# Optimization experiments

Hardware: AMD Instinct MI355X
Metric: run time of the kernel (lower is better)

The kernel has to match this reference:

```python
import jax, jax.numpy as jnp
import numpy as np
from jax import lax

B_, C_, H_, W_ = 4, 128, 64, 64
D_INNER, D_STATE, DT_RANK, D_CONV = 256, 16, 8, 4


def setup_inputs() -> dict:
    ks = jax.random.split(jax.random.key(0), 12)
    def rn(k, shape, fan_in):
        return jax.random.normal(k, shape, jnp.float32) * (fan_in ** -0.5)
    return {
        "x": jax.random.normal(ks[0], (B_, C_, H_, W_), jnp.float32),
        "proj_w": rn(ks[1], (C_, C_), C_),
        "in_proj_w": rn(ks[2], (2 * D_INNER, C_), C_),
        "conv_w": rn(ks[3], (D_INNER, 1, D_CONV), D_CONV),
        "conv_b": jax.random.normal(ks[4], (D_INNER,), jnp.float32) * 0.02,
        "x_proj_w": rn(ks[5], (DT_RANK + 2 * D_STATE, D_INNER), D_INNER),
        "dt_proj_w": rn(ks[6], (D_INNER, DT_RANK), DT_RANK),
        "dt_proj_b": jax.random.normal(ks[7], (D_INNER,), jnp.float32) * 0.1,
        "A_log": jax.random.uniform(ks[8], (D_INNER, D_STATE), jnp.float32),
        "D": jax.random.normal(ks[9], (D_INNER,), jnp.float32),
        "out_proj_w": rn(ks[10], (C_, D_INNER), D_INNER),
    }


def _mamba2d(x, proj_w, in_proj_w, conv_w, conv_b, x_proj_w, dt_proj_w, dt_proj_b, A_log, D, out_proj_w):
    b, c, h, w = x.shape
    L = h * w
    # 1x1 conv projection then flatten to sequence (b, L, c)
    u = jnp.einsum('oc,bchw->bohw', proj_w, x).reshape(b, c, L).transpose(0, 2, 1)
    # in_proj -> x, z gates
    xz = u @ in_proj_w.T                      # (b, L, 2*d_inner)
    xs, zg = xz[..., :D_INNER], xz[..., D_INNER:]
    # causal depthwise conv1d over sequence
    xt = xs.transpose(0, 2, 1)                # (b, d_inner, L)
    xt = lax.conv_general_dilated(xt, conv_w, window_strides=(1,),
                                  padding=[(D_CONV - 1, 0)],
                                  feature_group_count=D_INNER)
    xc = jax.nn.silu(xt + conv_b[None, :, None]).transpose(0, 2, 1)  # (b, L, d_inner)
    # input-dependent SSM params
    x_dbl = xc @ x_proj_w.T                   # (b, L, dt_rank + 2*d_state)
    dt_r = x_dbl[..., :DT_RANK]
    Bm = x_dbl[..., DT_RANK:DT_RANK + D_STATE]
    Cm = x_dbl[..., DT_RANK + D_STATE:]
    delta = jax.nn.softplus(dt_r @ dt_proj_w.T + dt_proj_b)  # (b, L, d_inner)
    A = -jnp.exp(A_log)                       # (d_inner, d_state)

    def step(hprev, inp):
        dt_t, B_t, C_t, x_t = inp             # (b,d), (b,n), (b,n), (b,d)
        dA = jnp.exp(dt_t[:, :, None] * A)    # (b, d, n)
        hn = dA * hprev + (dt_t * x_t)[:, :, None] * B_t[:, None, :]
        y = jnp.einsum('bdn,bn->bd', hn, C_t)
        return hn, y

    h0 = jnp.zeros((b, D_INNER, D_STATE), xc.dtype)
    _, ys = lax.scan(step, h0, (delta.transpose(1, 0, 2), Bm.transpose(1, 0, 2),
                                Cm.transpose(1, 0, 2), xc.transpose(1, 0, 2)))
    y = ys.transpose(1, 0, 2) + xc * D        # (b, L, d_inner) + skip
    y = y * jax.nn.silu(zg)                   # output gating
    out = y @ out_proj_w.T                    # (b, L, c)
    return out.transpose(0, 2, 1).reshape(b, c, h, w) + x


def reference(x, proj_w, in_proj_w, conv_w, conv_b, x_proj_w, dt_proj_w, dt_proj_b, A_log, D, out_proj_w):
    return _mamba2d(x, proj_w, in_proj_w, conv_w, conv_b, x_proj_w, dt_proj_w, dt_proj_b, A_log, D, out_proj_w)
```

## Files before the change

kernel.cpp:

```cpp
#include <hip/hip_runtime.h>


#define NCHUNK 128
#define CLEN 32

using s16x8 = __attribute__((ext_vector_type(8))) short;
using f32x4 = __attribute__((ext_vector_type(4))) float;

__device__ inline unsigned short f2bf(float f) {
  unsigned u = __float_as_uint(f);
  u = u + 0x7FFF + ((u >> 16) & 1);
  return (unsigned short)(u >> 16);
}

__global__ void prep_kernel(const float* __restrict__ proj_w,
                            const float* __restrict__ in_proj_w,
                            const float* __restrict__ x_proj_w,
                            const float* __restrict__ A_log,
                            unsigned short* __restrict__ W2b,
                            float* __restrict__ wT,
                            float* __restrict__ Aneg) {
  int idx = blockIdx.x * blockDim.x + threadIdx.x;
  if (idx < 512 * 128) {
    int o = idx >> 7, c = idx & 127;
    float acc = 0.f;
    #pragma unroll 4
    for (int i = 0; i < 128; ++i)
      acc += in_proj_w[o * 128 + i] * proj_w[i * 128 + c];
    W2b[idx] = f2bf(acc);
  } else if (idx < 512 * 128 + 256 * 40) {
    int t = idx - 512 * 128;
    int k = t / 40, j = t % 40;
    wT[t] = x_proj_w[j * 256 + k];
  } else if (idx < 512 * 128 + 256 * 40 + 256 * 16) {
    int t = idx - (512 * 128 + 256 * 40);
    Aneg[t] = -__expf(A_log[t]);
  }
}

__global__ __launch_bounds__(256, 1) void gemm_xz_kernel(
    const float* __restrict__ x, const unsigned short* __restrict__ W2b,
    float* __restrict__ xz) {
  __shared__ __align__(16) unsigned short At[128 * 128];
  __shared__ __align__(16) unsigned short Bt[256 * 128];
  int m0 = (blockIdx.x >> 1) * 128;
  int o0 = (blockIdx.x & 1) * 256;
  int b  = m0 >> 12;
  int l0 = m0 & 4095;
  int t = threadIdx.x;
  #pragma unroll
  for (int j = 0; j < 16; ++j) {
    int flat = t + j * 256;
    int cr = flat >> 5, lq = (flat & 31) << 2;
    float4 v = *reinterpret_cast<const float4*>(
        &x[((size_t)(b * 128 + cr)) * 4096 + l0 + lq]);
    float vv[4] = {v.x, v.y, v.z, v.w};
    #pragma unroll
    for (int e = 0; e < 4; ++e) {
      int l = lq + e;
      int g = (cr >> 3) ^ ((l & 7) << 1);
      At[l * 128 + g * 8 + (cr & 7)] = f2bf(vv[e]);
    }
  }
  #pragma unroll
  for (int j = 0; j < 16; ++j) {
    int flat = t + j * 256;
    int row = flat >> 4, gB = flat & 15;
    s16x8 v = *reinterpret_cast<const s16x8*>(&W2b[(size_t)(o0 + row) * 128 + gB * 8]);
    int g = gB ^ ((row & 7) << 1);
    *reinterpret_cast<s16x8*>(&Bt[row * 128 + g * 8]) = v;
  }
  __syncthreads();
  int ln = t & 63, wave = t >> 6;
  int wm = wave & 1, wn = wave >> 1;
  f32x4 acc[4][8] = {};
  #pragma unroll
  for (int ks = 0; ks < 4; ++ks) {
    int gk = ks * 4 + (ln >> 4);
    s16x8 a[4], bb[8];
    #pragma unroll
    for (int mi = 0; mi < 4; ++mi) {
      int lr = wm * 64 + mi * 16 + (ln & 15);
      a[mi] = *reinterpret_cast<const s16x8*>(&At[lr * 128 + (gk ^ ((lr & 7) << 1)) * 8]);
    }
    #pragma unroll
    for (int ni = 0; ni < 8; ++ni) {
      int orow = wn * 128 + ni * 16 + (ln & 15);
      bb[ni] = *reinterpret_cast<const s16x8*>(&Bt[orow * 128 + (gk ^ ((orow & 7) << 1)) * 8]);
    }
    #pragma unroll
    for (int mi = 0; mi < 4; ++mi)
      #pragma unroll
      for (int ni = 0; ni < 8; ++ni)
        acc[mi][ni] = __builtin_amdgcn_mfma_f32_16x16x32_bf16(a[mi], bb[ni], acc[mi][ni], 0, 0, 0);
  }
  #pragma unroll
  for (int mi = 0; mi < 4; ++mi)
    #pragma unroll
    for (int ni = 0; ni < 8; ++ni)
      #pragma unroll
      for (int r = 0; r < 4; ++r) {
        int row = wm * 64 + mi * 16 + (ln >> 4) * 4 + r;
        int col = wn * 128 + ni * 16 + (ln & 15);
        xz[(size_t)(m0 + row) * 512 + o0 + col] = acc[mi][ni][r];
      }
}

__global__ __launch_bounds__(256) void conv_silu_kernel(
    const float* __restrict__ xz, const float* __restrict__ conv_w,
    const float* __restrict__ conv_b, float* __restrict__ xc) {
  int bl0 = blockIdx.x * 8;
  int d = threadIdx.x;
  int l0 = bl0 & 4095;
  float w0 = conv_w[d * 4 + 0], w1 = conv_w[d * 4 + 1];
  float w2 = conv_w[d * 4 + 2], w3 = conv_w[d * 4 + 3];
  float cb = conv_b[d];
  float xm1 = (l0 >= 1) ? xz[(size_t)(bl0 - 1) * 512 + d] : 0.f;
  float xm2 = (l0 >= 2) ? xz[(size_t)(bl0 - 2) * 512 + d] : 0.f;
  float xm3 = (l0 >= 3) ? xz[(size_t)(bl0 - 3) * 512 + d] : 0.f;
  #pragma unroll
  for (int r = 0; r < 8; ++r) {
    size_t bl = bl0 + r;
    float x0 = xz[bl * 512 + d];
    float acc = cb + w3 * x0 + w2 * xm1 + w1 * xm2 + w0 * xm3;
    float s = acc * (1.f / (1.f + __expf(-acc)));
    xc[bl * 256 + d] = s;
    xm3 = xm2; xm2 = xm1; xm1 = x0;
  }
}

__global__ __launch_bounds__(256) void xdbl_scan1_kernel(
    const float* __restrict__ xc, const float* __restrict__ wT,
    const float* __restrict__ dt_proj_w, const float* __restrict__ dt_proj_b,
    const float* __restrict__ Aneg,
    float* __restrict__ BC, float* __restrict__ dlt,
    float* __restrict__ Ssum, float* __restrict__ chH) {
  __shared__ __align__(16) float lx[32][256];
  __shared__ float sdtr[32][8];
  __shared__ __align__(16) float lBC[32][32];
  int bc = blockIdx.x;
  int b = bc >> 7, c = bc & 127;
  int m0 = bc * 32;
  int tid = threadIdx.x;
  #pragma unroll
  for (int jj = 0; jj < 8; ++jj) {
    int i = tid + jj * 256;
    int row = i >> 6, colq = (i & 63) << 2;
    *reinterpret_cast<float4*>(&lx[row][colq]) =
        *reinterpret_cast<const float4*>(&xc[(size_t)(m0 + row) * 256 + colq]);
  }
  __syncthreads();
  {
    int j = tid & 63, g = tid >> 6;
    bool act = j < 40;
    float acc[8] = {};
    for (int k = 0; k < 256; ++k) {
      float w = act ? wT[k * 40 + j] : 0.f;
      #pragma unroll
      for (int i = 0; i < 8; ++i)
        acc[i] += lx[g * 8 + i][k] * w;
    }
    if (j < 8) {
      #pragma unroll
      for (int i = 0; i < 8; ++i)
        sdtr[g * 8 + i][j] = acc[i];
    } else if (j < 40) {
      #pragma unroll
      for (int i = 0; i < 8; ++i) {
        BC[(size_t)(m0 + g * 8 + i) * 32 + (j - 8)] = acc[i];
        lBC[g * 8 + i][j - 8] = acc[i];
      }
    }
  }
  __syncthreads();
  int d = tid;
  float dl_r[32];
  {
    float wrow[8];
    #pragma unroll
    for (int r = 0; r < 8; ++r) wrow[r] = dt_proj_w[d * 8 + r];
    float bb = dt_proj_b[d];
    #pragma unroll 4
    for (int r = 0; r < 32; ++r) {
      float a = bb;
      #pragma unroll
      for (int q = 0; q < 8; ++q) a += sdtr[r][q] * wrow[q];
      float sp = fmaxf(a, 0.f) + __logf(1.f + __expf(-fabsf(a)));
      dl_r[r] = sp;
      dlt[(size_t)(m0 + r) * 256 + d] = sp;
    }
  }
  float An[16];
  #pragma unroll
  for (int q = 0; q < 4; ++q)
    *reinterpret_cast<float4*>(&An[q * 4]) =
        *reinterpret_cast<const float4*>(&Aneg[d * 16 + q * 4]);
  float h[16] = {};
  float S = 0.f;
  #pragma unroll
  for (int t = 0; t < CLEN; ++t) {
    float dlv = dl_r[t];
    float dlx = dlv * lx[t][d];
    S += dlv;
    float4 B0 = *reinterpret_cast<const float4*>(&lBC[t][0]);
    float4 B1 = *reinterpret_cast<const float4*>(&lBC[t][4]);
    float4 B2 = *reinterpret_cast<const float4*>(&lBC[t][8]);
    float4 B3 = *reinterpret_cast<const float4*>(&lBC[t][12]);
    float Bv[16] = {B0.x,B0.y,B0.z,B0.w,B1.x,B1.y,B1.z,B1.w,
                    B2.x,B2.y,B2.z,B2.w,B3.x,B3.y,B3.z,B3.w};
    #pragma unroll
    for (int n = 0; n < 16; ++n)
      h[n] = __expf(dlv * An[n]) * h[n] + dlx * Bv[n];
  }
  int p = b * 256 + d;
  Ssum[c * 1024 + p] = S;
  size_t base = ((size_t)(c * 1024 + p)) * 16;
  #pragma unroll
  for (int q = 0; q < 4; ++q) {
    float4 v{h[q*4+0], h[q*4+1], h[q*4+2], h[q*4+3]};
    *reinterpret_cast<float4*>(&chH[base + q * 4]) = v;
  }
}

__global__ void scan2_kernel(const float* __restrict__ Aneg,
                             const float* __restrict__ Ssum,
                             const float* __restrict__ chH,
                             float* __restrict__ chS) {
  int q = blockIdx.x * blockDim.x + threadIdx.x;
  int p = q >> 4, n = q & 15;
  int d = p & 255;
  float An = Aneg[d * 16 + n];
  float h = 0.f;
  #pragma unroll 8
  for (int c = 0; c < NCHUNK; ++c) {
    size_t idx = ((size_t)(c * 1024 + p)) * 16 + n;
    float S = Ssum[c * 1024 + p];
    float hl = chH[idx];
    chS[idx] = h;
    h = __expf(An * S) * h + hl;
  }
}

__global__ __launch_bounds__(256) void scan3_kernel(
    const float* dlt, const float* __restrict__ xc,
    const float* __restrict__ BC, const float* __restrict__ Aneg,
    const float* __restrict__ chS, const float* __restrict__ Dvec,
    const float* __restrict__ xz, float* y2) {
  __shared__ __align__(16) float lBC[CLEN][32];
  int bc = blockIdx.x;
  int b = bc >> 7, c = bc & 127;
  int d = threadIdx.x;
  int bl0 = b * 4096 + c * CLEN;
  {
    int t = threadIdx.x >> 3, q = (threadIdx.x & 7) << 2;
    *reinterpret_cast<float4*>(&lBC[t][q]) =
        *reinterpret_cast<const float4*>(&BC[(size_t)(bl0 + t) * 32 + q]);
  }
  float An[16];
  #pragma unroll
  for (int q = 0; q < 4; ++q)
    *reinterpret_cast<float4*>(&An[q * 4]) =
        *reinterpret_cast<const float4*>(&Aneg[d * 16 + q * 4]);
  int p = b * 256 + d;
  float h[16];
  {
    size_t base = ((size_t)(c * 1024 + p)) * 16;
    #pragma unroll
    for (int q = 0; q < 4; ++q) {
      float4 v = *reinterpret_cast<const float4*>(&chS[base + q * 4]);
      h[q*4+0] = v.x; h[q*4+1] = v.y; h[q*4+2] = v.z; h[q*4+3] = v.w;
    }
  }
  float dl[CLEN], xv[CLEN], zv[CLEN];
  #pragma unroll
  for (int t = 0; t < CLEN; ++t) {
    dl[t] = dlt[(size_t)(bl0 + t) * 256 + d];
    xv[t] = xc[(size_t)(bl0 + t) * 256 + d];
    zv[t] = xz[(size_t)(bl0 + t) * 512 + 256 + d];
  }
  float Dd = Dvec[d];
  __syncthreads();
  #pragma unroll
  for (int t = 0; t < CLEN; ++t) {
    float dlv = dl[t];
    float xvv = xv[t];
    float dlx = dlv * xvv;
    float4 B0 = *reinterpret_cast<const float4*>(&lBC[t][0]);
    float4 B1 = *reinterpret_cast<const float4*>(&lBC[t][4]);
    float4 B2 = *reinterpret_cast<const float4*>(&lBC[t][8]);
    float4 B3 = *reinterpret_cast<const float4*>(&lBC[t][12]);
    float4 C0 = *reinterpret_cast<const float4*>(&lBC[t][16]);
    float4 C1 = *reinterpret_cast<const float4*>(&lBC[t][20]);
    float4 C2 = *reinterpret_cast<const float4*>(&lBC[t][24]);
    float4 C3 = *reinterpret_cast<const float4*>(&lBC[t][28]);
    float Bv[16] = {B0.x,B0.y,B0.z,B0.w,B1.x,B1.y,B1.z,B1.w,
                    B2.x,B2.y,B2.z,B2.w,B3.x,B3.y,B3.z,B3.w};
    float Cv[16] = {C0.x,C0.y,C0.z,C0.w,C1.x,C1.y,C1.z,C1.w,
                    C2.x,C2.y,C2.z,C2.w,C3.x,C3.y,C3.z,C3.w};
    float y = 0.f;
    #pragma unroll
    for (int n = 0; n < 16; ++n) {
      h[n] = __expf(dlv * An[n]) * h[n] + dlx * Bv[n];
      y += h[n] * Cv[n];
    }
    float z = zv[t];
    float sil = z * (1.f / (1.f + __expf(-z)));
    y2[(size_t)(bl0 + t) * 256 + d] = (y + xvv * Dd) * sil;
  }
}

__global__ __launch_bounds__(256) void gemm_out_kernel(
    const float* __restrict__ y2, const float* __restrict__ Wout,
    const float* __restrict__ x, float* __restrict__ out) {
  __shared__ __align__(16) float ys[64][68];
  __shared__ __align__(16) float ws2[64][132];
  int m0 = blockIdx.x * 64;
  int b = m0 >> 12;
  int l0 = m0 & 4095;
  int tid = threadIdx.x;
  int tx = tid & 7;
  int ty = tid >> 3;
  float acc[8][4] = {};
  for (int kc = 0; kc < 256; kc += 64) {
    #pragma unroll
    for (int jj = 0; jj < 4; ++jj) {
      int i = tid + jj * 256;
      int ml = i >> 4, kq = (i & 15) << 2;
      float4 v = *reinterpret_cast<const float4*>(
          &y2[(size_t)(m0 + ml) * 256 + kc + kq]);
      ys[kq + 0][ml] = v.x; ys[kq + 1][ml] = v.y;
      ys[kq + 2][ml] = v.z; ys[kq + 3][ml] = v.w;
    }
    #pragma unroll
    for (int jj = 0; jj < 8; ++jj) {
      int i = tid + jj * 256;
      int cc = i >> 4, kq = (i & 15) << 2;
      float4 v = *reinterpret_cast<const float4*>(&Wout[(size_t)cc * 256 + kc + kq]);
      ws2[kq + 0][cc] = v.x; ws2[kq + 1][cc] = v.y;
      ws2[kq + 2][cc] = v.z; ws2[kq + 3][cc] = v.w;
    }
    __syncthreads();
    for (int kk = 0; kk < 64; ++kk) {
      float4 xa = *reinterpret_cast<const float4*>(&ys[kk][tx * 8]);
      float4 xb = *reinterpret_cast<const float4*>(&ys[kk][tx * 8 + 4]);
      float4 wa = *reinterpret_cast<const float4*>(&ws2[kk][ty * 4]);
      float xv[8] = {xa.x, xa.y, xa.z, xa.w, xb.x, xb.y, xb.z, xb.w};
      float wv[4] = {wa.x, wa.y, wa.z, wa.w};
      #pragma unroll
      for (int i2 = 0; i2 < 8; ++i2)
        #pragma unroll
        for (int j2 = 0; j2 < 4; ++j2)
          acc[i2][j2] += xv[i2] * wv[j2];
    }
    __syncthreads();
  }
  #pragma unroll
  for (int j2 = 0; j2 < 4; ++j2) {
    int cc = ty * 4 + j2;
    size_t base = ((size_t)(b * 128 + cc)) * 4096 + l0 + tx * 8;
    float4 xa = *reinterpret_cast<const float4*>(&x[base]);
    float4 xb = *reinterpret_cast<const float4*>(&x[base + 4]);
    float4 r0{acc[0][j2] + xa.x, acc[1][j2] + xa.y, acc[2][j2] + xa.z, acc[3][j2] + xa.w};
    float4 r1{acc[4][j2] + xb.x, acc[5][j2] + xb.y, acc[6][j2] + xb.z, acc[7][j2] + xb.w};
    *reinterpret_cast<float4*>(&out[base]) = r0;
    *reinterpret_cast<float4*>(&out[base + 4]) = r1;
  }
}

extern "C" void kernel_launch(void* const* d_in, const int* in_sizes, int n_in,
                              void* d_out, int out_size, void* d_ws, size_t ws_size,
                              hipStream_t stream) {
  const float* x         = (const float*)d_in[0];
  const float* proj_w    = (const float*)d_in[1];
  const float* in_proj_w = (const float*)d_in[2];
  const float* conv_w    = (const float*)d_in[3];
  const float* conv_b    = (const float*)d_in[4];
  const float* x_proj_w  = (const float*)d_in[5];
  const float* dt_proj_w = (const float*)d_in[6];
  const float* dt_proj_b = (const float*)d_in[7];
  const float* A_log     = (const float*)d_in[8];
  const float* Dvec      = (const float*)d_in[9];
  const float* out_proj_w= (const float*)d_in[10];

  float* ws   = (float*)d_ws;
  float* wT   = ws;
  float* Aneg = wT + 10240;
  unsigned short* W2b = (unsigned short*)(Aneg + 4096);
  float* xz   = Aneg + 4096 + 32768;
  float* xc   = xz + 8388608;
  float* BC   = xc + 4194304;
  float* dlt  = BC + 524288;
  float* Ssum = dlt + 4194304;
  float* chH  = Ssum + 131072;
  float* chS  = chH + 2097152;
  float* y2   = dlt;
  float* out  = (float*)d_out;

  prep_kernel<<<312, 256, 0, stream>>>(proj_w, in_proj_w, x_proj_w, A_log, W2b, wT, Aneg);
  gemm_xz_kernel<<<256, 256, 0, stream>>>(x, W2b, xz);
  conv_silu_kernel<<<2048, 256, 0, stream>>>(xz, conv_w, conv_b, xc);
  xdbl_scan1_kernel<<<512, 256, 0, stream>>>(xc, wT, dt_proj_w, dt_proj_b, Aneg,
                                             BC, dlt, Ssum, chH);
  scan2_kernel<<<64, 256, 0, stream>>>(Aneg, Ssum, chH, chS);
  scan3_kernel<<<512, 256, 0, stream>>>(dlt, xc, BC, Aneg, chS, Dvec, xz, y2);
  gemm_out_kernel<<<256, 256, 0, stream>>>(y2, out_proj_w, x, out);
}
```

Before: 220.1 us.

## Move x_proj and out_proj GEMMs to bf16 MFMA and recompute delta in scans

Splits the x_proj projection out of the first scan kernel into a bf16 MFMA GEMM, which needs a bf16 copy of xc written by the conv kernel. The out_proj GEMM moves from an fp32 FMA tile loop to MFMA on bf16 y2 and bf16 weights. Delta is no longer stored; both scan passes recompute it from the small dt_r values, which removes a large fp32 intermediate write and read. The cost is an extra launch, extra bf16 rounding on activations, and duplicated softplus work in both scans.

```diff
diff --git a/kernel.cpp b/kernel.cpp
--- a/kernel.cpp
+++ b/kernel.cpp
@@ -16,24 +16,29 @@
 __global__ void prep_kernel(const float* __restrict__ proj_w,
                             const float* __restrict__ in_proj_w,
                             const float* __restrict__ x_proj_w,
+                            const float* __restrict__ out_proj_w,
                             const float* __restrict__ A_log,
                             unsigned short* __restrict__ W2b,
-                            float* __restrict__ wT,
+                            unsigned short* __restrict__ wTb48,
+                            unsigned short* __restrict__ Woutb,
                             float* __restrict__ Aneg) {
   int idx = blockIdx.x * blockDim.x + threadIdx.x;
-  if (idx < 512 * 128) {
+  if (idx < 65536) {
     int o = idx >> 7, c = idx & 127;
     float acc = 0.f;
     #pragma unroll 4
     for (int i = 0; i < 128; ++i)
       acc += in_proj_w[o * 128 + i] * proj_w[i * 128 + c];
     W2b[idx] = f2bf(acc);
-  } else if (idx < 512 * 128 + 256 * 40) {
-    int t = idx - 512 * 128;
-    int k = t / 40, j = t % 40;
-    wT[t] = x_proj_w[j * 256 + k];
-  } else if (idx < 512 * 128 + 256 * 40 + 256 * 16) {
-    int t = idx - (512 * 128 + 256 * 40);
+  } else if (idx < 65536 + 12288) {
+    int t = idx - 65536;
+    int j = t >> 8, k = t & 255;
+    wTb48[t] = (j < 40) ? f2bf(x_proj_w[j * 256 + k]) : (unsigned short)0;
+  } else if (idx < 65536 + 12288 + 32768) {
+    int t = idx - (65536 + 12288);
+    Woutb[t] = f2bf(out_proj_w[t]);
+  } else if (idx < 65536 + 12288 + 32768 + 4096) {
+    int t = idx - (65536 + 12288 + 32768);
     Aneg[t] = -__expf(A_log[t]);
   }
 }
@@ -108,7 +113,8 @@
 
 __global__ __launch_bounds__(256) void conv_silu_kernel(
     const float* __restrict__ xz, const float* __restrict__ conv_w,
-    const float* __restrict__ conv_b, float* __restrict__ xc) {
+    const float* __restrict__ conv_b, float* __restrict__ xc,
+    unsigned short* __restrict__ xcb) {
   int bl0 = blockIdx.x * 8;
   int d = threadIdx.x;
   int l0 = bl0 & 4095;
@@ -125,83 +131,106 @@
     float acc = cb + w3 * x0 + w2 * xm1 + w1 * xm2 + w0 * xm3;
     float s = acc * (1.f / (1.f + __expf(-acc)));
     xc[bl * 256 + d] = s;
+    xcb[bl * 256 + d] = f2bf(s);
     xm3 = xm2; xm2 = xm1; xm1 = x0;
   }
 }
 
-__global__ __launch_bounds__(256) void xdbl_scan1_kernel(
-    const float* __restrict__ xc, const float* __restrict__ wT,
+__global__ __launch_bounds__(256) void xdbl_mfma_kernel(
+    const unsigned short* __restrict__ xcb, const unsigned short* __restrict__ wTb48,
+    float* __restrict__ xdbl48) {
+  __shared__ __align__(16) unsigned short At[64 * 256];
+  __shared__ __align__(16) unsigned short Bt[48 * 256];
+  int m0 = blockIdx.x * 64;
+  int t = threadIdx.x;
+  #pragma unroll
+  for (int it = 0; it < 8; ++it) {
+    int f = t + it * 256;
+    int row = f >> 5, g0 = f & 31;
+    s16x8 v = *reinterpret_cast<const s16x8*>(&xcb[(size_t)(m0 + row) * 256 + g0 * 8]);
+    int g = g0 ^ ((row & 7) << 1);
+    *reinterpret_cast<s16x8*>(&At[row * 256 + g * 8]) = v;
+  }
+  #pragma unroll
+  for (int it = 0; it < 6; ++it) {
+    int f = t + it * 256;
+    int row = f >> 5, g0 = f & 31;
+    s16x8 v = *reinterpret_cast<const s16x8*>(&wTb48[(size_t)row * 256 + g0 * 8]);
+    int g = g0 ^ ((row & 7) << 1);
+    *reinterpret_cast<s16x8*>(&Bt[row * 256 + g * 8]) = v;
+  }
+  __syncthreads();
+  int ln = t & 63, wm = t >> 6;
+  f32x4 acc[3] = {};
+  #pragma unroll
+  for (int ks = 0; ks < 8; ++ks) {
+    int gk = ks * 4 + (ln >> 4);
+    int ar = wm * 16 + (ln & 15);
+    s16x8 a = *reinterpret_cast<const s16x8*>(&At[ar * 256 + (gk ^ ((ar & 7) << 1)) * 8]);
+    #pragma unroll
+    for (int nt = 0; nt < 3; ++nt) {
+      int br = nt * 16 + (ln & 15);
+      s16x8 bb = *reinterpret_cast<const s16x8*>(&Bt[br * 256 + (gk ^ ((br & 7) << 1)) * 8]);
+      acc[nt] = __builtin_amdgcn_mfma_f32_16x16x32_bf16(a, bb, acc[nt], 0, 0, 0);
+    }
+  }
+  #pragma unroll
+  for (int nt = 0; nt < 3; ++nt)
+    #pragma unroll
+    for (int r = 0; r < 4; ++r) {
+      int row = m0 + wm * 16 + (ln >> 4) * 4 + r;
+      xdbl48[(size_t)row * 48 + nt * 16 + (ln & 15)] = acc[nt][r];
+    }
+}
+
+__global__ __launch_bounds__(256) void scan1_kernel(
+    const float* __restrict__ xc, const float* __restrict__ xdbl48,
     const float* __restrict__ dt_proj_w, const float* __restrict__ dt_proj_b,
     const float* __restrict__ Aneg,
-    float* __restrict__ BC, float* __restrict__ dlt,
     float* __restrict__ Ssum, float* __restrict__ chH) {
-  __shared__ __align__(16) float lx[32][256];
-  __shared__ float sdtr[32][8];
-  __shared__ __align__(16) float lBC[32][32];
+  __shared__ __align__(16) float lBC[CLEN][32];
+  __shared__ __align__(16) float sdtr[CLEN][8];
   int bc = blockIdx.x;
-  int b = bc >> 7, c = bc & 127;
-  int m0 = bc * 32;
+  int b = bc >> 7;
+  int bl0 = bc * 32;
   int tid = threadIdx.x;
-  #pragma unroll
-  for (int jj = 0; jj < 8; ++jj) {
-    int i = tid + jj * 256;
-    int row = i >> 6, colq = (i & 63) << 2;
-    *reinterpret_cast<float4*>(&lx[row][colq]) =
-        *reinterpret_cast<const float4*>(&xc[(size_t)(m0 + row) * 256 + colq]);
-  }
-  __syncthreads();
   {
-    int j = tid & 63, g = tid >> 6;
-    bool act = j < 40;
-    float acc[8] = {};
-    for (int k = 0; k < 256; ++k) {
-      float w = act ? wT[k * 40 + j] : 0.f;
-      #pragma unroll
-      for (int i = 0; i < 8; ++i)
-        acc[i] += lx[g * 8 + i][k] * w;
-    }
-    if (j < 8) {
-      #pragma unroll
-      for (int i = 0; i < 8; ++i)
-        sdtr[g * 8 + i][j] = acc[i];
-    } else if (j < 40) {
-      #pragma unroll
-      for (int i = 0; i < 8; ++i) {
-        BC[(size_t)(m0 + g * 8 + i) * 32 + (j - 8)] = acc[i];
-        lBC[g * 8 + i][j - 8] = acc[i];
-      }
-    }
-  }
-  __syncthreads();
+    int t0 = tid >> 3, q = (tid & 7) << 2;
+    *reinterpret_cast<float4*>(&lBC[t0][q]) =
+        *reinterpret_cast<const float4*>(&xdbl48[(size_t)(bl0 + t0) * 48 + 8 + q]);
+    if (tid < 64) {
+      int t1 = tid >> 1, q1 = (tid & 1) << 2;
+      *reinterpret_cast<float4*>(&sdtr[t1][q1]) =
+          *reinterpret_cast<const float4*>(&xdbl48[(size_t)(bl0 + t1) * 48 + q1]);
+    }
+  }
   int d = tid;
-  float dl_r[32];
-  {
-    float wrow[8];
-    #pragma unroll
-    for (int r = 0; r < 8; ++r) wrow[r] = dt_proj_w[d * 8 + r];
-    float bb = dt_proj_b[d];
-    #pragma unroll 4
-    for (int r = 0; r < 32; ++r) {
-      float a = bb;
-      #pragma unroll
-      for (int q = 0; q < 8; ++q) a += sdtr[r][q] * wrow[q];
-      float sp = fmaxf(a, 0.f) + __logf(1.f + __expf(-fabsf(a)));
-      dl_r[r] = sp;
-      dlt[(size_t)(m0 + r) * 256 + d] = sp;
-    }
-  }
+  float wrow[8];
+  *reinterpret_cast<float4*>(&wrow[0]) =
+      *reinterpret_cast<const float4*>(&dt_proj_w[d * 8]);
+  *reinterpret_cast<float4*>(&wrow[4]) =
+      *reinterpret_cast<const float4*>(&dt_proj_w[d * 8 + 4]);
+  float bb = dt_proj_b[d];
   float An[16];
   #pragma unroll
   for (int q = 0; q < 4; ++q)
     *reinterpret_cast<float4*>(&An[q * 4]) =
         *reinterpret_cast<const float4*>(&Aneg[d * 16 + q * 4]);
+  float xv[CLEN];
+  #pragma unroll
+  for (int t = 0; t < CLEN; ++t)
+    xv[t] = xc[(size_t)(bl0 + t) * 256 + d];
+  __syncthreads();
   float h[16] = {};
   float S = 0.f;
   #pragma unroll
   for (int t = 0; t < CLEN; ++t) {
-    float dlv = dl_r[t];
-    float dlx = dlv * lx[t][d];
+    float a = bb;
+    #pragma unroll
+    for (int q = 0; q < 8; ++q) a += sdtr[t][q] * wrow[q];
+    float dlv = fmaxf(a, 0.f) + __logf(1.f + __expf(-fabsf(a)));
     S += dlv;
+    float dlx = dlv * xv[t];
     float4 B0 = *reinterpret_cast<const float4*>(&lBC[t][0]);
     float4 B1 = *reinterpret_cast<const float4*>(&lBC[t][4]);
     float4 B2 = *reinterpret_cast<const float4*>(&lBC[t][8]);
@@ -212,6 +241,7 @@
     for (int n = 0; n < 16; ++n)
       h[n] = __expf(dlv * An[n]) * h[n] + dlx * Bv[n];
   }
+  int c = bc & 127;
   int p = b * 256 + d;
   Ssum[c * 1024 + p] = S;
   size_t base = ((size_t)(c * 1024 + p)) * 16;
@@ -242,20 +272,34 @@
 }
 
 __global__ __launch_bounds__(256) void scan3_kernel(
-    const float* dlt, const float* __restrict__ xc,
-    const float* __restrict__ BC, const float* __restrict__ Aneg,
-    const float* __restrict__ chS, const float* __restrict__ Dvec,
-    const float* __restrict__ xz, float* y2) {
+    const float* __restrict__ xc, const float* __restrict__ xdbl48,
+    const float* __restrict__ dt_proj_w, const float* __restrict__ dt_proj_b,
+    const float* __restrict__ Aneg, const float* __restrict__ chS,
+    const float* __restrict__ Dvec, const float* __restrict__ xz,
+    unsigned short* __restrict__ y2b) {
   __shared__ __align__(16) float lBC[CLEN][32];
+  __shared__ __align__(16) float sdtr[CLEN][8];
   int bc = blockIdx.x;
   int b = bc >> 7, c = bc & 127;
-  int d = threadIdx.x;
-  int bl0 = b * 4096 + c * CLEN;
+  int bl0 = bc * 32;
+  int tid = threadIdx.x;
   {
-    int t = threadIdx.x >> 3, q = (threadIdx.x & 7) << 2;
-    *reinterpret_cast<float4*>(&lBC[t][q]) =
-        *reinterpret_cast<const float4*>(&BC[(size_t)(bl0 + t) * 32 + q]);
-  }
+    int t0 = tid >> 3, q = (tid & 7) << 2;
+    *reinterpret_cast<float4*>(&lBC[t0][q]) =
+        *reinterpret_cast<const float4*>(&xdbl48[(size_t)(bl0 + t0) * 48 + 8 + q]);
+    if (tid < 64) {
+      int t1 = tid >> 1, q1 = (tid & 1) << 2;
+      *reinterpret_cast<float4*>(&sdtr[t1][q1]) =
+          *reinterpret_cast<const float4*>(&xdbl48[(size_t)(bl0 + t1) * 48 + q1]);
+    }
+  }
+  int d = tid;
+  float wrow[8];
+  *reinterpret_cast<float4*>(&wrow[0]) =
+      *reinterpret_cast<const float4*>(&dt_proj_w[d * 8]);
+  *reinterpret_cast<float4*>(&wrow[4]) =
+      *reinterpret_cast<const float4*>(&dt_proj_w[d * 8 + 4]);
+  float bb = dt_proj_b[d];
   float An[16];
   #pragma unroll
   for (int q = 0; q < 4; ++q)
@@ -271,10 +315,9 @@
       h[q*4+0] = v.x; h[q*4+1] = v.y; h[q*4+2] = v.z; h[q*4+3] = v.w;
     }
   }
-  float dl[CLEN], xv[CLEN], zv[CLEN];
+  float xv[CLEN], zv[CLEN];
   #pragma unroll
   for (int t = 0; t < CLEN; ++t) {
-    dl[t] = dlt[(size_t)(bl0 + t) * 256 + d];
     xv[t] = xc[(size_t)(bl0 + t) * 256 + d];
     zv[t] = xz[(size_t)(bl0 + t) * 512 + 256 + d];
   }
@@ -282,7 +325,10 @@
   __syncthreads();
   #pragma unroll
   for (int t = 0; t < CLEN; ++t) {
-    float dlv = dl[t];
+    float a = bb;
+    #pragma unroll
+    for (int q = 0; q < 8; ++q) a += sdtr[t][q] * wrow[q];
+    float dlv = fmaxf(a, 0.f) + __logf(1.f + __expf(-fabsf(a)));
     float xvv = xv[t];
     float dlx = dlv * xvv;
     float4 B0 = *reinterpret_cast<const float4*>(&lBC[t][0]);
@@ -305,65 +351,56 @@
     }
     float z = zv[t];
     float sil = z * (1.f / (1.f + __expf(-z)));
-    y2[(size_t)(bl0 + t) * 256 + d] = (y + xvv * Dd) * sil;
+    y2b[(size_t)(bl0 + t) * 256 + d] = f2bf((y + xvv * Dd) * sil);
   }
 }
 
 __global__ __launch_bounds__(256) void gemm_out_kernel(
-    const float* __restrict__ y2, const float* __restrict__ Wout,
+    const unsigned short* __restrict__ y2b, const unsigned short* __restrict__ Woutb,
     const float* __restrict__ x, float* __restrict__ out) {
-  __shared__ __align__(16) float ys[64][68];
-  __shared__ __align__(16) float ws2[64][132];
+  __shared__ __align__(16) unsigned short At[64 * 256];
+  __shared__ __align__(16) unsigned short Bt[128 * 256];
   int m0 = blockIdx.x * 64;
-  int b = m0 >> 12;
-  int l0 = m0 & 4095;
-  int tid = threadIdx.x;
-  int tx = tid & 7;
-  int ty = tid >> 3;
-  float acc[8][4] = {};
-  for (int kc = 0; kc < 256; kc += 64) {
-    #pragma unroll
-    for (int jj = 0; jj < 4; ++jj) {
-      int i = tid + jj * 256;
-      int ml = i >> 4, kq = (i & 15) << 2;
-      float4 v = *reinterpret_cast<const float4*>(
-          &y2[(size_t)(m0 + ml) * 256 + kc + kq]);
-      ys[kq + 0][ml] = v.x; ys[kq + 1][ml] = v.y;
-      ys[kq + 2][ml] = v.z; ys[kq + 3][ml] = v.w;
-    }
-    #pragma unroll
-    for (int jj = 0; jj < 8; ++jj) {
-      int i = tid + jj * 256;
-      int cc = i >> 4, kq = (i & 15) << 2;
-      float4 v = *reinterpret_cast<const float4*>(&Wout[(size_t)cc * 256 + kc + kq]);
-      ws2[kq + 0][cc] = v.x; ws2[kq + 1][cc] = v.y;
-      ws2[kq + 2][cc] = v.z; ws2[kq + 3][cc] = v.w;
-    }
-    __syncthreads();
-    for (int kk = 0; kk < 64; ++kk) {
-      float4 xa = *reinterpret_cast<const float4*>(&ys[kk][tx * 8]);
-      float4 xb = *reinterpret_cast<const float4*>(&ys[kk][tx * 8 + 4]);
-      float4 wa = *reinterpret_cast<const float4*>(&ws2[kk][ty * 4]);
-      float xv[8] = {xa.x, xa.y, xa.z, xa.w, xb.x, xb.y, xb.z, xb.w};
-      float wv[4] = {wa.x, wa.y, wa.z, wa.w};
-      #pragma unroll
-      for (int i2 = 0; i2 < 8; ++i2)
-        #pragma unroll
-        for (int j2 = 0; j2 < 4; ++j2)
-          acc[i2][j2] += xv[i2] * wv[j2];
-    }
-    __syncthreads();
-  }
-  #pragma unroll
-  for (int j2 = 0; j2 < 4; ++j2) {
-    int cc = ty * 4 + j2;
-    size_t base = ((size_t)(b * 128 + cc)) * 4096 + l0 + tx * 8;
-    float4 xa = *reinterpret_cast<const float4*>(&x[base]);
-    float4 xb = *reinterpret_cast<const float4*>(&x[base + 4]);
-    float4 r0{acc[0][j2] + xa.x, acc[1][j2] + xa.y, acc[2][j2] + xa.z, acc[3][j2] + xa.w};
-    float4 r1{acc[4][j2] + xb.x, acc[5][j2] + xb.y, acc[6][j2] + xb.z, acc[7][j2] + xb.w};
-    *reinterpret_cast<float4*>(&out[base]) = r0;
-    *reinterpret_cast<float4*>(&out[base + 4]) = r1;
+  int b = m0 >> 12, l0 = m0 & 4095;
+  int t = threadIdx.x;
+  #pragma unroll
+  for (int it = 0; it < 8; ++it) {
+    int f = t + it * 256;
+    int row = f >> 5, g0 = f & 31;
+    s16x8 v = *reinterpret_cast<const s16x8*>(&y2b[(size_t)(m0 + row) * 256 + g0 * 8]);
+    int g = g0 ^ ((row & 7) << 1);
+    *reinterpret_cast<s16x8*>(&At[row * 256 + g * 8]) = v;
+  }
+  #pragma unroll
+  for (int it = 0; it < 16; ++it) {
+    int f = t + it * 256;
+    int row = f >> 5, g0 = f & 31;
+    s16x8 v = *reinterpret_cast<const s16x8*>(&Woutb[(size_t)row * 256 + g0 * 8]);
+    int g = g0 ^ ((row & 7) << 1);
+    *reinterpret_cast<s16x8*>(&Bt[row * 256 + g * 8]) = v;
+  }
+  __syncthreads();
+  int ln = t & 63, wm = t >> 6;
+  f32x4 acc[8] = {};
+  #pragma unroll
+  for (int ks = 0; ks < 8; ++ks) {
+    int gk = ks * 4 + (ln >> 4);
+    int ar = wm * 16 + (ln & 15);
+    s16x8 a = *reinterpret_cast<const s16x8*>(&At[ar * 256 + (gk ^ ((ar & 7) << 1)) * 8]);
+    #pragma unroll
+    for (int nt = 0; nt < 8; ++nt) {
+      int br = nt * 16 + (ln & 15);
+      s16x8 bb = *reinterpret_cast<const s16x8*>(&Bt[br * 256 + (gk ^ ((br & 7) << 1)) * 8]);
+      acc[nt] = __builtin_amdgcn_mfma_f32_16x16x32_bf16(a, bb, acc[nt], 0, 0, 0);
+    }
+  }
+  #pragma unroll
+  for (int nt = 0; nt < 8; ++nt) {
+    int cc = nt * 16 + (ln & 15);
+    size_t base = ((size_t)(b * 128 + cc)) * 4096 + l0 + wm * 16 + ((ln >> 4) << 2);
+    float4 xr = *reinterpret_cast<const float4*>(&x[base]);
+    float4 o{acc[nt][0] + xr.x, acc[nt][1] + xr.y, acc[nt][2] + xr.z, acc[nt][3] + xr.w};
+    *reinterpret_cast<float4*>(&out[base]) = o;
   }
 }
 
@@ -382,26 +419,29 @@
   const float* Dvec      = (const float*)d_in[9];
   const float* out_proj_w= (const float*)d_in[10];
 
-  float* ws   = (float*)d_ws;
-  float* wT   = ws;
-  float* Aneg = wT + 10240;
-  unsigned short* W2b = (unsigned short*)(Aneg + 4096);
-  float* xz   = Aneg + 4096 + 32768;
-  float* xc   = xz + 8388608;
-  float* BC   = xc + 4194304;
-  float* dlt  = BC + 524288;
-  float* Ssum = dlt + 4194304;
-  float* chH  = Ssum + 131072;
-  float* chS  = chH + 2097152;
-  float* y2   = dlt;
-  float* out  = (float*)d_out;
-
-  prep_kernel<<<312, 256, 0, stream>>>(proj_w, in_proj_w, x_proj_w, A_log, W2b, wT, Aneg);
+  float* ws = (float*)d_ws;
+  float*          Aneg   = ws;
+  unsigned short* W2b    = (unsigned short*)(ws + 4096);
+  unsigned short* wTb48  = (unsigned short*)(ws + 36864);
+  unsigned short* Woutb  = (unsigned short*)(ws + 43008);
+  float*          xz     = ws + 59392;
+  float*          xc     = xz + 8388608;
+  unsigned short* xcb    = (unsigned short*)(xc + 4194304);
+  float*          xdbl48 = xc + 4194304 + 2097152;
+  float*          Ssum   = xdbl48 + 786432;
+  float*          chH    = Ssum + 131072;
+  float*          chS    = chH + 2097152;
+  unsigned short* y2b    = (unsigned short*)(chS + 2097152);
+  float* out = (float*)d_out;
+
+  prep_kernel<<<448, 256, 0, stream>>>(proj_w, in_proj_w, x_proj_w, out_proj_w, A_log,
+                                       W2b, wTb48, Woutb, Aneg);
   gemm_xz_kernel<<<256, 256, 0, stream>>>(x, W2b, xz);
-  conv_silu_kernel<<<2048, 256, 0, stream>>>(xz, conv_w, conv_b, xc);
-  xdbl_scan1_kernel<<<512, 256, 0, stream>>>(xc, wT, dt_proj_w, dt_proj_b, Aneg,
-                                             BC, dlt, Ssum, chH);
+  conv_silu_kernel<<<2048, 256, 0, stream>>>(xz, conv_w, conv_b, xc, xcb);
+  xdbl_mfma_kernel<<<256, 256, 0, stream>>>(xcb, wTb48, xdbl48);
+  scan1_kernel<<<512, 256, 0, stream>>>(xc, xdbl48, dt_proj_w, dt_proj_b, Aneg, Ssum, chH);
   scan2_kernel<<<64, 256, 0, stream>>>(Aneg, Ssum, chH, chS);
-  scan3_kernel<<<512, 256, 0, stream>>>(dlt, xc, BC, Aneg, chS, Dvec, xz, y2);
-  gemm_out_kernel<<<256, 256, 0, stream>>>(y2, out_proj_w, x, out);
-}
+  scan3_kernel<<<512, 256, 0, stream>>>(xc, xdbl48, dt_proj_w, dt_proj_b, Aneg, chS,
+                                        Dvec, xz, y2b);
+  gemm_out_kernel<<<256, 256, 0, stream>>>(y2b, Woutb, x, out);
+}
```

New measurement: 185.0 us. -15.9%, faster.
